# Kernel optimization log

Measured on AMD Instinct MI355X. Metric: run time of the kernel, lower is better.

## Reference

```python
import jax, jax.numpy as jnp
import numpy as np

DIM = 2048
NUM_EXPERTS = 64
TOPK = 8
ROUTE_SCALE = 1.0


def setup_inputs() -> dict:
    key = jax.random.key(0)
    kx, kw = jax.random.split(key)
    x = jax.random.normal(kx, (16384, DIM), dtype=jnp.float32)
    # xavier_uniform_ for weight of shape (num_experts, dim)
    limit = float(np.sqrt(6.0 / (NUM_EXPERTS + DIM)))
    weight = jax.random.uniform(kw, (NUM_EXPERTS, DIM), dtype=jnp.float32,
                                minval=-limit, maxval=limit)
    bias = jnp.zeros((NUM_EXPERTS,), dtype=jnp.float32)
    return {"x": x, "weight": weight, "bias": bias}


def reference(x, weight, bias):
    # logits: (N, E) = x @ weight.T + bias
    logits = jnp.einsum('nd,ed->ne', x, weight) + bias
    probs = jax.nn.softmax(logits * ROUTE_SCALE, axis=-1)
    topk_vals, topk_idx = jax.lax.top_k(probs, TOPK)  # (N, topk) each
    # dense gate: scatter topk_vals into (N, num_experts)
    N = x.shape[0]
    dense_gate = jnp.zeros((N, NUM_EXPERTS), dtype=probs.dtype)
    rows = jnp.arange(N)[:, None]
    dense_gate = dense_gate.at[rows, topk_idx].set(topk_vals)
    return topk_vals, topk_idx, dense_gate
```

## Files before the change

### kernel.cpp

```cpp
#include <hip/hip_runtime.h>
#include <math.h>

#pragma clang fp contract(off)


#define NROWS 16384
#define DIM   2048
#define NE    64
#define MARGIN 1e-4f
#define MAXCAND 12
#define WS_WOFF (512 * 1024)

typedef float f32x4 __attribute__((ext_vector_type(4)));
typedef short s16x8 __attribute__((ext_vector_type(8)));

__device__ __forceinline__ void ld16_lds(const float* g, void* l) {
  __builtin_amdgcn_global_load_lds((const __attribute__((address_space(1))) void*)g,
                                   (__attribute__((address_space(3))) void*)l, 16, 0, 0);
}
__device__ __forceinline__ unsigned short bf16_rne(float f) {
  unsigned u = __builtin_bit_cast(unsigned, f);
  u += 0x7FFFu + ((u >> 16) & 1u);
  return (unsigned short)(u >> 16);
}
__device__ __forceinline__ float bf16f(unsigned short h) {
  return __builtin_bit_cast(float, (unsigned)h << 16);
}
__device__ __forceinline__ void cvt8(const f32x4 a, const f32x4 b, s16x8* hi, s16x8* lo) {
#pragma unroll
  for (int j = 0; j < 4; ++j) {
    unsigned short h = bf16_rne(a[j]);
    (*hi)[j] = (short)h; (*lo)[j] = (short)bf16_rne(a[j] - bf16f(h));
  }
#pragma unroll
  for (int j = 0; j < 4; ++j) {
    unsigned short h = bf16_rne(b[j]);
    (*hi)[4 + j] = (short)h; (*lo)[4 + j] = (short)bf16_rne(b[j] - bf16f(h));
  }
}

__global__ __launch_bounds__(256, 8)
void w_split(const float* __restrict__ w, unsigned short* __restrict__ whf,
             unsigned short* __restrict__ wlf) {
  const int i = blockIdx.x * 256 + threadIdx.x;
  const int e = i >> 11, k = i & 2047;
  float v = w[i];
  unsigned short h = bf16_rne(v);
  unsigned short lo = bf16_rne(v - bf16f(h));
  const int n = e >> 4, col = e & 15;
  const int kt = k >> 5, j = k & 31;
  const int lane = col | ((j >> 3) << 4);
  const size_t off = (((size_t)(kt << 2) + n) * 64 + lane) * 8 + (j & 7);
  whf[off] = h; wlf[off] = lo;
}

__global__ void zero_flags(int* __restrict__ flags) {
  if (threadIdx.x == 0) flags[0] = 0;
}

template <bool USE_WS>
__global__ __launch_bounds__(512, 2)
void mfma_logits(const float* __restrict__ x, const float* __restrict__ w,
                 const float* __restrict__ bias, float* __restrict__ lg,
                 const unsigned short* __restrict__ whf,
                 const unsigned short* __restrict__ wlf)
{
  __shared__ float part[8][64][33];

  const int t = threadIdx.x;
  const int wv = t >> 6, lane = t & 63;
  const int rowBase = blockIdx.x << 6;
  const int frow = lane & 15;
  const int fk   = (lane >> 4) << 3;
  const size_t q0 = (size_t)wv * 256;

  const float* xb0 = x + (size_t)(rowBase + frow) * DIM + q0 + fk;
  const float* xb1 = xb0 + (size_t)16 * DIM;
  const float* xb2 = xb0 + (size_t)32 * DIM;
  const float* xb3 = xb0 + (size_t)48 * DIM;
  const float* wb = w + (size_t)frow * DIM + q0 + fk;
  const int ktg0 = wv << 3;

  f32x4 acc[4][4];
#pragma unroll
  for (int m = 0; m < 4; ++m)
#pragma unroll
    for (int n = 0; n < 4; ++n) acc[m][n] = (f32x4)(0.f);

#pragma unroll 1
  for (int kt = 0; kt < 8; ++kt) {
    const int ko = kt << 5;
    s16x8 ah[4], al[4];
    {
      f32x4 a0, a1;
      a0 = *(const f32x4*)(xb0 + ko); a1 = *(const f32x4*)(xb0 + ko + 4);
      cvt8(a0, a1, &ah[0], &al[0]);
      a0 = *(const f32x4*)(xb1 + ko); a1 = *(const f32x4*)(xb1 + ko + 4);
      cvt8(a0, a1, &ah[1], &al[1]);
      a0 = *(const f32x4*)(xb2 + ko); a1 = *(const f32x4*)(xb2 + ko + 4);
      cvt8(a0, a1, &ah[2], &al[2]);
      a0 = *(const f32x4*)(xb3 + ko); a1 = *(const f32x4*)(xb3 + ko + 4);
      cvt8(a0, a1, &ah[3], &al[3]);
    }
#pragma unroll
    for (int n = 0; n < 4; ++n) {
      s16x8 bh, bl;
      if constexpr (USE_WS) {
        const size_t foff = (((size_t)((ktg0 + kt) << 2) + n) * 64 + lane) * 8;
        bh = *(const s16x8*)(whf + foff);
        bl = *(const s16x8*)(wlf + foff);
      } else {
        const float* wp = wb + (size_t)(n << 4) * DIM + ko;
        f32x4 b0 = *(const f32x4*)(wp);
        f32x4 b1 = *(const f32x4*)(wp + 4);
        cvt8(b0, b1, &bh, &bl);
      }
#pragma unroll
      for (int m = 0; m < 4; ++m) {
        acc[m][n] = __builtin_amdgcn_mfma_f32_16x16x32_bf16(al[m], bh, acc[m][n], 0, 0, 0);
        acc[m][n] = __builtin_amdgcn_mfma_f32_16x16x32_bf16(ah[m], bl, acc[m][n], 0, 0, 0);
        acc[m][n] = __builtin_amdgcn_mfma_f32_16x16x32_bf16(ah[m], bh, acc[m][n], 0, 0, 0);
      }
    }
  }

#pragma unroll
  for (int ph = 0; ph < 2; ++ph) {
    if (ph) __syncthreads();
#pragma unroll
    for (int mm = 0; mm < 2; ++mm) {
      const int m = (ph << 1) + mm;
#pragma unroll
      for (int n = 0; n < 4; ++n)
#pragma unroll
        for (int r = 0; r < 4; ++r)
          part[wv][(n << 4) + (lane & 15)][(mm << 4) + ((lane >> 4) << 2) + r] = acc[m][n][r];
    }
    __syncthreads();
#pragma unroll
    for (int i = t; i < 2048; i += 512) {
      const int row = i >> 6, col = i & 63;
      float v = ((part[0][col][row] + part[1][col][row])
               + (part[2][col][row] + part[3][col][row]))
              + ((part[4][col][row] + part[5][col][row])
               + (part[6][col][row] + part[7][col][row]));
      lg[(size_t)(rowBase + (ph << 5) + row) * NE + col] = v + bias[col];
    }
  }
}

__global__ __launch_bounds__(256, 4)
void finish_kernel(float* __restrict__ gate, float* __restrict__ out_vals,
                   float* __restrict__ out_idx, int* __restrict__ flags, int maxf)
{
  const int t    = threadIdx.x;
  const int row  = blockIdx.x * 4 + (t >> 6);
  const int lane = t & 63;

  float l = gate[(size_t)row * NE + lane];

  float m = l;
#pragma unroll
  for (int d = 32; d >= 1; d >>= 1) m = fmaxf(m, __shfl_xor(m, d));
  float pe = expf(l - m);
  float s = pe;
#pragma unroll
  for (int d = 32; d >= 1; d >>= 1) s = s + __shfl_xor(s, d);
  float p = pe / s;

  float cur = l;
  float sval[9]; int sidx[9];
  unsigned long long used8 = 0;
#pragma unroll
  for (int k = 0; k < 9; ++k) {
    float v = cur; int i = lane;
#pragma unroll
    for (int d = 1; d < 64; d <<= 1) {
      float ov = __shfl_xor(v, d);
      int   oi = __shfl_xor(i, d);
      bool take = (ov > v) || (ov == v && oi < i);
      v = take ? ov : v;
      i = take ? oi : i;
    }
    sval[k] = v; sidx[k] = i;
    if (k < 8) {
      used8 |= 1ull << i;
      if (lane == i) cur = -INFINITY;
    }
  }

  float myv = 0.f, myi = 0.f;
#pragma unroll
  for (int k = 0; k < 8; ++k) {
    float pv = __shfl(p, sidx[k]);
    if (lane == k) { myv = pv; myi = (float)sidx[k]; }
  }
  if (lane < 8) {
    out_vals[(size_t)row * 8 + lane] = myv;
    out_idx [(size_t)row * 8 + lane] = myi;
  }

  gate[(size_t)row * NE + lane] = ((used8 >> lane) & 1ull) ? p : 0.0f;

  float ming = INFINITY;
#pragma unroll
  for (int k = 1; k < 9; ++k) ming = fminf(ming, sval[k - 1] - sval[k]);
  if (ming < MARGIN && maxf > 0) {
    unsigned long long cmask = __ballot(l >= sval[7] - MARGIN);
    int n = __popcll(cmask);
    if (n <= MAXCAND) {
      int slot = 0;
      if (lane == 0) slot = atomicAdd(flags, 1);
      slot = __shfl(slot, 0);
      if (slot < maxf) {
        int* rec = flags + 4 + slot * 32;
        if (lane == 0) { rec[0] = row; rec[1] = n; }
        if ((cmask >> lane) & 1ull) {
          int pos = __popcll(cmask & ((1ull << lane) - 1ull));
          rec[2 + pos] = lane;
          ((float*)(rec + 14))[pos] = p;
        }
      }
    }
  }
}

__global__ __launch_bounds__(64, 1)
void exact_fix(const float* __restrict__ x, const float* __restrict__ w,
               const float* __restrict__ bias, const int* __restrict__ flags,
               int maxf, float* __restrict__ out_vals, float* __restrict__ out_idx,
               float* __restrict__ gate)
{
  __shared__ float xs_[DIM];
  __shared__ float wl_[MAXCAND * DIM];
  __shared__ float exl[MAXCAND];

  int count = flags[0]; if (count > maxf) count = maxf;
  const int lane = threadIdx.x;

  for (int recI = blockIdx.x; recI < count; recI += (int)gridDim.x) {
    const int* rec = flags + 4 + recI * 32;
    const int row = rec[0], n = rec[1];

#pragma unroll
    for (int i = 0; i < 8; ++i)
      ld16_lds(x + (size_t)row * DIM + i * 256 + lane * 4, &xs_[i * 256 + lane * 4]);
    for (int c = 0; c < n; ++c)
#pragma unroll
      for (int i = 0; i < 8; ++i)
        ld16_lds(w + (size_t)rec[2 + c] * DIM + i * 256 + lane * 4,
                 &wl_[c * DIM + i * 256 + lane * 4]);
    asm volatile("s_waitcnt vmcnt(0)" ::: "memory");
    __builtin_amdgcn_s_barrier();

    const int c = lane >> 2, jj = lane & 3;
    const int cw = (c < n) ? c : 0;
    const float* wrow = &wl_[cw * DIM];
    float a = 0.f;
#pragma unroll 4
    for (int b = 0; b < 128; ++b) {
      const int k = (b << 4) + jj;
      a = a + xs_[k + 12] * wrow[k + 12];
      a = a + xs_[k + 8]  * wrow[k + 8];
      a = a + xs_[k + 4]  * wrow[k + 4];
      a = a + xs_[k]      * wrow[k];
    }
    float o1 = __shfl_xor(a, 1);
    float s01 = a + o1;
    float o2 = __shfl_xor(s01, 2);
    float tot = (s01 + o2) + bias[rec[2 + cw]];
    if (jj == 0 && c < n) exl[c] = tot;
    __syncthreads();

    if (lane == 0) {
      unsigned used = 0;
      const float* cp = (const float*)(rec + 14);
      for (int k = 0; k < 8; ++k) {
        float best = -INFINITY; int bi = 0;
        for (int c2 = 0; c2 < n; ++c2) {
          bool ok = (((used >> c2) & 1u) == 0u) && (exl[c2] > best);
          best = ok ? exl[c2] : best;
          bi   = ok ? c2      : bi;
        }
        used |= 1u << bi;
        out_vals[(size_t)row * 8 + k] = cp[bi];
        out_idx [(size_t)row * 8 + k] = (float)rec[2 + bi];
      }
      for (int c2 = 0; c2 < n; ++c2)
        gate[(size_t)row * NE + rec[2 + c2]] = ((used >> c2) & 1u) ? cp[c2] : 0.f;
    }
    __syncthreads();
  }
}

extern "C" void kernel_launch(void* const* d_in, const int* in_sizes, int n_in,
                              void* d_out, int out_size, void* d_ws, size_t ws_size,
                              hipStream_t stream) {
  const float* x    = (const float*)d_in[0];
  const float* w    = (const float*)d_in[1];
  const float* bias = (const float*)d_in[2];
  float* out   = (float*)d_out;
  float* vals  = out;
  float* idx   = out + (size_t)NROWS * 8;
  float* dense = out + (size_t)NROWS * 16;
  (void)in_sizes; (void)n_in; (void)out_size;

  const bool use_ws_w = ws_size >= WS_WOFF + (size_t)NE * DIM * 4;
  int maxf = 0;
  if (ws_size >= 16 + 32 * 4) {
    size_t cap = (ws_size / 4 - 4) / 32;
    if (cap > 2048) cap = 2048;
    if (use_ws_w) { size_t cap2 = (WS_WOFF / 4 - 4) / 32; if (cap > cap2) cap = cap2; }
    maxf = (int)cap;
  }
  int* flags = (int*)d_ws;
  unsigned short* whf = (unsigned short*)((char*)d_ws + WS_WOFF);
  unsigned short* wlf = whf + (size_t)NE * DIM;

  if (use_ws_w) {
    w_split<<<dim3(NE * DIM / 256), dim3(256), 0, stream>>>(w, whf, wlf);
    mfma_logits<true><<<dim3(NROWS / 64), dim3(512), 0, stream>>>(x, w, bias, dense, whf, wlf);
  } else {
    mfma_logits<false><<<dim3(NROWS / 64), dim3(512), 0, stream>>>(x, w, bias, dense, whf, wlf);
  }
  if (maxf > 0) zero_flags<<<dim3(1), dim3(64), 0, stream>>>(flags);
  finish_kernel<<<dim3(NROWS / 4), dim3(256), 0, stream>>>(dense, vals, idx, flags, maxf);
  if (maxf > 0)
    exact_fix<<<dim3(128), dim3(64), 0, stream>>>(x, w, bias, flags, maxf, vals, idx, dense);
}
```

Before: 91.39 us.

## Split K across 16 waves per block and interleave A loads in pairs

```diff
diff --git a/kernel.cpp b/kernel.cpp
--- a/kernel.cpp
+++ b/kernel.cpp
@@ -59,27 +59,27 @@
 }
 
 template <bool USE_WS>
-__global__ __launch_bounds__(512, 2)
+__global__ __launch_bounds__(1024, 1)
 void mfma_logits(const float* __restrict__ x, const float* __restrict__ w,
                  const float* __restrict__ bias, float* __restrict__ lg,
                  const unsigned short* __restrict__ whf,
                  const unsigned short* __restrict__ wlf)
 {
-  __shared__ float part[8][64][33];
+  __shared__ float part[16][64][33];
 
   const int t = threadIdx.x;
   const int wv = t >> 6, lane = t & 63;
   const int rowBase = blockIdx.x << 6;
   const int frow = lane & 15;
   const int fk   = (lane >> 4) << 3;
-  const size_t q0 = (size_t)wv * 256;
-
-  const float* xb0 = x + (size_t)(rowBase + frow) * DIM + q0 + fk;
-  const float* xb1 = xb0 + (size_t)16 * DIM;
-  const float* xb2 = xb0 + (size_t)32 * DIM;
-  const float* xb3 = xb0 + (size_t)48 * DIM;
+  const size_t q0 = (size_t)wv * 128;
+
+  const float* xb[4];
+#pragma unroll
+  for (int m = 0; m < 4; ++m)
+    xb[m] = x + (size_t)(rowBase + (m << 4) + frow) * DIM + q0 + fk;
   const float* wb = w + (size_t)frow * DIM + q0 + fk;
-  const int ktg0 = wv << 3;
+  const int ktg0 = wv << 2;
 
   f32x4 acc[4][4];
 #pragma unroll
@@ -88,38 +88,40 @@
     for (int n = 0; n < 4; ++n) acc[m][n] = (f32x4)(0.f);
 
 #pragma unroll 1
-  for (int kt = 0; kt < 8; ++kt) {
+  for (int kt = 0; kt < 4; ++kt) {
     const int ko = kt << 5;
-    s16x8 ah[4], al[4];
-    {
-      f32x4 a0, a1;
-      a0 = *(const f32x4*)(xb0 + ko); a1 = *(const f32x4*)(xb0 + ko + 4);
-      cvt8(a0, a1, &ah[0], &al[0]);
-      a0 = *(const f32x4*)(xb1 + ko); a1 = *(const f32x4*)(xb1 + ko + 4);
-      cvt8(a0, a1, &ah[1], &al[1]);
-      a0 = *(const f32x4*)(xb2 + ko); a1 = *(const f32x4*)(xb2 + ko + 4);
-      cvt8(a0, a1, &ah[2], &al[2]);
-      a0 = *(const f32x4*)(xb3 + ko); a1 = *(const f32x4*)(xb3 + ko + 4);
-      cvt8(a0, a1, &ah[3], &al[3]);
-    }
-#pragma unroll
-    for (int n = 0; n < 4; ++n) {
-      s16x8 bh, bl;
-      if constexpr (USE_WS) {
-        const size_t foff = (((size_t)((ktg0 + kt) << 2) + n) * 64 + lane) * 8;
-        bh = *(const s16x8*)(whf + foff);
-        bl = *(const s16x8*)(wlf + foff);
-      } else {
-        const float* wp = wb + (size_t)(n << 4) * DIM + ko;
-        f32x4 b0 = *(const f32x4*)(wp);
-        f32x4 b1 = *(const f32x4*)(wp + 4);
-        cvt8(b0, b1, &bh, &bl);
+#pragma unroll
+    for (int mp = 0; mp < 2; ++mp) {
+      s16x8 ah0, al0, ah1, al1;
+      {
+        f32x4 a0, a1;
+        a0 = *(const f32x4*)(xb[2 * mp] + ko);
+        a1 = *(const f32x4*)(xb[2 * mp] + ko + 4);
+        cvt8(a0, a1, &ah0, &al0);
+        a0 = *(const f32x4*)(xb[2 * mp + 1] + ko);
+        a1 = *(const f32x4*)(xb[2 * mp + 1] + ko + 4);
+        cvt8(a0, a1, &ah1, &al1);
       }
 #pragma unroll
-      for (int m = 0; m < 4; ++m) {
-        acc[m][n] = __builtin_amdgcn_mfma_f32_16x16x32_bf16(al[m], bh, acc[m][n], 0, 0, 0);
-        acc[m][n] = __builtin_amdgcn_mfma_f32_16x16x32_bf16(ah[m], bl, acc[m][n], 0, 0, 0);
-        acc[m][n] = __builtin_amdgcn_mfma_f32_16x16x32_bf16(ah[m], bh, acc[m][n], 0, 0, 0);
+      for (int n = 0; n < 4; ++n) {
+        s16x8 bh, bl;
+        if constexpr (USE_WS) {
+          const size_t foff = (((size_t)((ktg0 + kt) << 2) + n) * 64 + lane) * 8;
+          bh = *(const s16x8*)(whf + foff);
+          bl = *(const s16x8*)(wlf + foff);
+        } else {
+          const float* wp = wb + (size_t)(n << 4) * DIM + ko;
+          f32x4 b0 = *(const f32x4*)(wp);
+          f32x4 b1 = *(const f32x4*)(wp + 4);
+          cvt8(b0, b1, &bh, &bl);
+        }
+        const int m0 = 2 * mp, m1 = 2 * mp + 1;
+        acc[m0][n] = __builtin_amdgcn_mfma_f32_16x16x32_bf16(al0, bh, acc[m0][n], 0, 0, 0);
+        acc[m0][n] = __builtin_amdgcn_mfma_f32_16x16x32_bf16(ah0, bl, acc[m0][n], 0, 0, 0);
+        acc[m0][n] = __builtin_amdgcn_mfma_f32_16x16x32_bf16(ah0, bh, acc[m0][n], 0, 0, 0);
+        acc[m1][n] = __builtin_amdgcn_mfma_f32_16x16x32_bf16(al1, bh, acc[m1][n], 0, 0, 0);
+        acc[m1][n] = __builtin_amdgcn_mfma_f32_16x16x32_bf16(ah1, bl, acc[m1][n], 0, 0, 0);
+        acc[m1][n] = __builtin_amdgcn_mfma_f32_16x16x32_bf16(ah1, bh, acc[m1][n], 0, 0, 0);
       }
     }
   }
@@ -138,13 +140,17 @@
     }
     __syncthreads();
 #pragma unroll
-    for (int i = t; i < 2048; i += 512) {
+    for (int i = t; i < 2048; i += 1024) {
       const int row = i >> 6, col = i & 63;
-      float v = ((part[0][col][row] + part[1][col][row])
-               + (part[2][col][row] + part[3][col][row]))
-              + ((part[4][col][row] + part[5][col][row])
-               + (part[6][col][row] + part[7][col][row]));
-      lg[(size_t)(rowBase + (ph << 5) + row) * NE + col] = v + bias[col];
+      float v0 = ((part[0][col][row] + part[1][col][row])
+                + (part[2][col][row] + part[3][col][row]))
+               + ((part[4][col][row] + part[5][col][row])
+                + (part[6][col][row] + part[7][col][row]));
+      float v1 = ((part[8][col][row] + part[9][col][row])
+                + (part[10][col][row] + part[11][col][row]))
+               + ((part[12][col][row] + part[13][col][row])
+                + (part[14][col][row] + part[15][col][row]));
+      lg[(size_t)(rowBase + (ph << 5) + row) * NE + col] = (v0 + v1) + bias[col];
     }
   }
 }
@@ -319,9 +325,9 @@
 
   if (use_ws_w) {
     w_split<<<dim3(NE * DIM / 256), dim3(256), 0, stream>>>(w, whf, wlf);
-    mfma_logits<true><<<dim3(NROWS / 64), dim3(512), 0, stream>>>(x, w, bias, dense, whf, wlf);
+    mfma_logits<true><<<dim3(NROWS / 64), dim3(1024), 0, stream>>>(x, w, bias, dense, whf, wlf);
   } else {
-    mfma_logits<false><<<dim3(NROWS / 64), dim3(512), 0, stream>>>(x, w, bias, dense, whf, wlf);
+    mfma_logits<false><<<dim3(NROWS / 64), dim3(1024), 0, stream>>>(x, w, bias, dense, whf, wlf);
   }
   if (maxf > 0) zero_flags<<<dim3(1), dim3(64), 0, stream>>>(flags);
   finish_kernel<<<dim3(NROWS / 4), dim3(256), 0, stream>>>(dense, vals, idx, flags, maxf);
```

New measurement: 97.81 us. 1.07x slower.
